# Kernel optimization log

Hardware: AMD Instinct MI355X
Metric: run time of the kernel (lower is better)

The kernel has to match this reference:

```python
import jax, jax.numpy as jnp
import numpy as np

POOL = 7
H, W, C = 200, 200, 512
NUM_ROIS = 128


def setup_inputs() -> dict:
    key = jax.random.key(0)
    k1, k2, k3 = jax.random.split(key, 3)
    img = jax.random.normal(k1, (1, H, W, C), dtype=jnp.float32)
    # (x, y, w, h) in feature-map pixels; w,h >= POOL+1 so every bin is >=1px,
    # and x+w <= W, y+h <= H so crops stay in bounds (as the original assumes).
    wh = jax.random.uniform(k2, (1, NUM_ROIS, 2), minval=float(POOL + 1), maxval=64.0)
    xy = jax.random.uniform(k3, (1, NUM_ROIS, 2)) * (jnp.array([W, H], jnp.float32) - wh)
    rois = jnp.concatenate([xy, wh], axis=-1).astype(jnp.float32)
    return {"img": img, "rois": rois, "pool_size": POOL}


def _roi_pool(x, rois, P):
    # x: (H, W, C) feature map; rois: (R, 4) as (x, y, w, h) floats.
    h_dim, w_dim, _ = x.shape
    ks = jnp.arange(P + 1, dtype=jnp.float32)
    rows = jnp.arange(h_dim)
    cols = jnp.arange(w_dim)

    def pool_one(roi):
        rx, ry, rw, rh = roi[0], roi[1], roi[2], roi[3]
        # Bin boundaries: original computes x1 = int(x + ix*w/P), x2 = int(x + (ix+1)*w/P),
        # i.e. contiguous non-overlapping segments [b[k], b[k+1]).
        bx = (rx + ks * (rw / P)).astype(jnp.int32)
        by = (ry + ks * (rh / P)).astype(jnp.int32)
        # Map each row/col to its bin id; out-of-roi pixels -> dummy segment P.
        rid = jnp.searchsorted(by, rows, side='right') - 1
        rid = jnp.where((rid < 0) | (rid >= P), P, rid)
        cid = jnp.searchsorted(bx, cols, side='right') - 1
        cid = jnp.where((cid < 0) | (cid >= P), P, cid)
        # Max-reduce rows into y-bins, then cols into x-bins (separable rect max).
        rm = jax.ops.segment_max(x, rid, num_segments=P + 1)                     # (P+1, W, C) [jy, w, c]
        cm = jax.ops.segment_max(rm.transpose(1, 0, 2), cid, num_segments=P + 1)  # (P+1, P+1, C) [ix, jy, c]
        return cm[:P, :P].transpose(1, 0, 2)  # (jy, ix, c)

    return jax.vmap(pool_one)(rois)  # (R, P, P, C)


def reference(img, rois, pool_size):
    # Output: (1, num_rois, pool_size, pool_size, channels), tf dim ordering.
    out = _roi_pool(img[0], rois[0], pool_size)
    return out[None]
```

## Files before the change

### kernel.cpp

```cpp
#include <hip/hip_runtime.h>


#define IMG_H 200
#define IMG_W 200
#define IMG_C 512
#define C4 (IMG_C / 4)
#define POOL 7
#define NROI 128
#define PLANES 4
#define NXCD 8
#define NBIN (POOL * POOL)
#define ROIS_PER_XCD (NROI / NXCD)

typedef float f4v __attribute__((ext_vector_type(4)));

__device__ __forceinline__ float4 max4(float4 a, float4 b) {
    return make_float4(fmaxf(a.x, b.x), fmaxf(a.y, b.y),
                       fmaxf(a.z, b.z), fmaxf(a.w, b.w));
}

__device__ __forceinline__ unsigned spread8(unsigned x) {
    x &= 0xFFu;
    x = (x | (x << 4)) & 0x0F0Fu;
    x = (x | (x << 2)) & 0x3333u;
    x = (x | (x << 1)) & 0x5555u;
    return x;
}

__global__ __launch_bounds__(PLANES * 128, 8) void roi_pool_kernel(
    const float* __restrict__ img,
    const float* __restrict__ rois,
    float* __restrict__ out)
{
    __shared__ unsigned short s_key[NROI];
    __shared__ int s_roi;
    __shared__ float4 red[PLANES - 1][C4];

    const int tid = threadIdx.x;

    const int xcd  = blockIdx.x & (NXCD - 1);
    const int ixcd = blockIdx.x >> 3;
    const int rank = xcd * ROIS_PER_XCD + ixcd / NBIN;
    const int bin  = ixcd % NBIN;

    if (tid < NROI) {
        const float rx = rois[tid * 4 + 0];
        const float ry = rois[tid * 4 + 1];
        const float rw = rois[tid * 4 + 2];
        const float rh = rois[tid * 4 + 3];
        const unsigned cx = (unsigned)(int)(rx + 0.5f * rw);
        const unsigned cy = (unsigned)(int)(ry + 0.5f * rh);
        s_key[tid] = (unsigned short)((spread8(cy) << 1) | spread8(cx));
    }
    __syncthreads();
    if (tid < NROI) {
        const unsigned my = s_key[tid];
        int r = 0;
        #pragma unroll 8
        for (int u = 0; u < NROI; ++u) {
            const unsigned ku = s_key[u];
            r += (int)((ku < my) | ((ku == my) & (u < tid)));
        }
        if (r == rank) s_roi = tid;
    }
    __syncthreads();
    const int roi = s_roi;

    const int jy = bin / POOL;
    const int ix = bin % POOL;

    const float rx = rois[roi * 4 + 0];
    const float ry = rois[roi * 4 + 1];
    const float rw = rois[roi * 4 + 2];
    const float rh = rois[roi * 4 + 3];

    const float sx = __fdiv_rn(rw, 7.0f);
    const float sy = __fdiv_rn(rh, 7.0f);
    const int x1 = (int)__fadd_rn(rx, __fmul_rn((float)ix,       sx));
    const int x2 = (int)__fadd_rn(rx, __fmul_rn((float)(ix + 1), sx));
    const int y1 = (int)__fadd_rn(ry, __fmul_rn((float)jy,       sy));
    const int y2 = (int)__fadd_rn(ry, __fmul_rn((float)(jy + 1), sy));

    const int c4 = tid & 127;
    const int p  = tid >> 7;
    const float4* __restrict__ img4 = (const float4*)img;

    const int bw = x2 - x1;
    const int bh = y2 - y1;
    const int area = bw * bh;
    (void)bh;

    const float4 NEG = make_float4(-INFINITY, -INFINITY, -INFINITY, -INFINITY);
    float4 m = NEG;

    int dx = p, dy = 0;
    while (dx >= bw) { dx -= bw; ++dy; }
    #pragma unroll 2
    for (int i = p; i < area; i += PLANES) {
        const size_t px = (size_t)(y1 + dy) * IMG_W + (size_t)(x1 + dx);
        m = max4(m, img4[px * C4 + c4]);
        dx += PLANES;
        while (dx >= bw) { dx -= bw; ++dy; }
    }

    if (p > 0) red[p - 1][c4] = m;
    __syncthreads();
    if (p == 0) {
        m = max4(m, red[0][c4]);
        m = max4(m, red[1][c4]);
        m = max4(m, red[2][c4]);

        float4* __restrict__ out4 = (float4*)out;
        f4v* __restrict__ dst =
            (f4v*)&out4[((size_t)(roi * POOL + jy) * POOL + ix) * C4 + c4];
        __builtin_nontemporal_store(*(const f4v*)&m, dst);
    }
}

extern "C" void kernel_launch(void* const* d_in, const int* in_sizes, int n_in,
                              void* d_out, int out_size, void* d_ws, size_t ws_size,
                              hipStream_t stream) {
    (void)in_sizes; (void)n_in; (void)d_ws; (void)ws_size; (void)out_size;
    const float* img  = (const float*)d_in[0];
    const float* rois = (const float*)d_in[1];
    float* out = (float*)d_out;

    dim3 grid(NROI * NBIN);
    dim3 block(PLANES * 128);
    roi_pool_kernel<<<grid, block, 0, stream>>>(img, rois, out);
}
```

Measured before the change: 153.1 us.

## Balance ROI work across XCDs by area-weighted Morton-ordered chunking

Result: faster. 145.1 us (-5.2%).

```diff
diff --git a/kernel.cpp b/kernel.cpp
--- a/kernel.cpp
+++ b/kernel.cpp
@@ -10,7 +10,8 @@
 #define PLANES 4
 #define NXCD 8
 #define NBIN (POOL * POOL)
-#define ROIS_PER_XCD (NROI / NXCD)
+#define NITEM (NROI * NBIN)
+#define SLOTS_PER_XCD (NITEM / NXCD)
 
 typedef float f4v __attribute__((ext_vector_type(4)));
 
@@ -18,6 +19,9 @@
     return make_float4(fmaxf(a.x, b.x), fmaxf(a.y, b.y),
                        fmaxf(a.z, b.z), fmaxf(a.w, b.w));
 }
+
+__device__ __forceinline__ int imin(int a, int b) { return a < b ? a : b; }
+__device__ __forceinline__ int imax(int a, int b) { return a > b ? a : b; }
 
 __device__ __forceinline__ unsigned spread8(unsigned x) {
     x &= 0xFFu;
@@ -33,39 +37,119 @@
     float* __restrict__ out)
 {
     __shared__ unsigned short s_key[NROI];
-    __shared__ int s_roi;
-    __shared__ float4 red[PLANES - 1][C4];
+    __shared__ float          s_areaROI[NROI];
+    __shared__ int            s_rank[NROI];
+    __shared__ unsigned char  s_perm[NROI];
+    __shared__ float          s_area[NROI];
+    __shared__ float          s_pref[NROI];
+    __shared__ int            s_chunk[NROI];
+    __shared__ int            s_rstart[NXCD];
+    __shared__ int            s_len[NXCD];
+    __shared__ int            s_spillpre[NXCD + 1];
+    __shared__ int            s_freepre[NXCD + 1];
+    __shared__ int            s_roi, s_bin;
+    __shared__ float4         red[PLANES - 1][C4];
 
     const int tid = threadIdx.x;
-
-    const int xcd  = blockIdx.x & (NXCD - 1);
-    const int ixcd = blockIdx.x >> 3;
-    const int rank = xcd * ROIS_PER_XCD + ixcd / NBIN;
-    const int bin  = ixcd % NBIN;
-
-    if (tid < NROI) {
-        const float rx = rois[tid * 4 + 0];
-        const float ry = rois[tid * 4 + 1];
-        const float rw = rois[tid * 4 + 2];
-        const float rh = rois[tid * 4 + 3];
+    const int t   = tid & 127;
+    const int seg = tid >> 7;
+
+    if (seg == 0) {
+        const float rx = rois[t * 4 + 0];
+        const float ry = rois[t * 4 + 1];
+        const float rw = rois[t * 4 + 2];
+        const float rh = rois[t * 4 + 3];
         const unsigned cx = (unsigned)(int)(rx + 0.5f * rw);
         const unsigned cy = (unsigned)(int)(ry + 0.5f * rh);
-        s_key[tid] = (unsigned short)((spread8(cy) << 1) | spread8(cx));
-    }
-    __syncthreads();
-    if (tid < NROI) {
-        const unsigned my = s_key[tid];
+        s_key[t] = (unsigned short)((spread8(cy) << 1) | spread8(cx));
+        s_areaROI[t] = rw * rh;
+        s_rank[t] = 0;
+    }
+    if (tid < NXCD) s_len[tid] = 0;
+    __syncthreads();
+
+    {
+        const unsigned my = s_key[t];
         int r = 0;
+        const int u0 = seg * 32;
         #pragma unroll 8
-        for (int u = 0; u < NROI; ++u) {
+        for (int u = u0; u < u0 + 32; ++u) {
             const unsigned ku = s_key[u];
-            r += (int)((ku < my) | ((ku == my) & (u < tid)));
-        }
-        if (r == rank) s_roi = tid;
-    }
-    __syncthreads();
+            r += (int)((ku < my) | ((ku == my) & (u < t)));
+        }
+        atomicAdd(&s_rank[t], r);
+    }
+    __syncthreads();
+
+    if (seg == 0) {
+        const int r = s_rank[t];
+        s_perm[r] = (unsigned char)t;
+        s_area[r] = s_areaROI[t];
+    }
+    __syncthreads();
+
+    if (seg == 0) {
+        float v = s_area[t];
+        #pragma unroll
+        for (int d = 1; d < 64; d <<= 1) {
+            const float o = __shfl_up(v, d);
+            if ((t & 63) >= d) v += o;
+        }
+        s_pref[t] = v;
+    }
+    __syncthreads();
+
+    if (seg == 0) {
+        const float w0tot = s_pref[63];
+        const float pre   = s_pref[t] + ((t >= 64) ? w0tot : 0.f);
+        const float total = s_pref[127] + w0tot;
+        const float mid = pre - 0.5f * s_area[t];
+        const int c = imin((int)(mid * ((float)NXCD / total)), NXCD - 1);
+        s_chunk[t] = c;
+        atomicAdd(&s_len[c], NBIN);
+    }
+    __syncthreads();
+
+    if (seg == 0) {
+        const int c = s_chunk[t];
+        if (t == 0 || s_chunk[t - 1] != c) s_rstart[c] = t;
+    }
+    if (tid == 0) {
+        int sp = 0, fp = 0;
+        #pragma unroll
+        for (int x = 0; x < NXCD; ++x) {
+            s_spillpre[x] = sp;
+            s_freepre[x]  = fp;
+            sp += imax(0, s_len[x] - SLOTS_PER_XCD);
+            fp += imax(0, SLOTS_PER_XCD - s_len[x]);
+        }
+        s_spillpre[NXCD] = sp;
+        s_freepre[NXCD]  = fp;
+    }
+    __syncthreads();
+
+    if (tid == 0) {
+        const int x = blockIdx.x & (NXCD - 1);
+        const int j = blockIdx.x >> 3;
+        int tt, mm;
+        if (j < s_len[x]) {
+            tt = s_rstart[x] + j / NBIN;
+            mm = j % NBIN;
+        } else {
+            const int si = s_freepre[x] + (j - s_len[x]);
+            int xx = 0;
+            while (!(si >= s_spillpre[xx] && si < s_spillpre[xx + 1])) ++xx;
+            const int jj = SLOTS_PER_XCD + (si - s_spillpre[xx]);
+            tt = s_rstart[xx] + jj / NBIN;
+            mm = jj % NBIN;
+        }
+        s_roi = (int)s_perm[tt];
+        s_bin = mm;
+    }
+    __syncthreads();
+
     const int roi = s_roi;
-
+    const int bin = s_bin;
     const int jy = bin / POOL;
     const int ix = bin % POOL;
 
@@ -86,9 +170,7 @@
     const float4* __restrict__ img4 = (const float4*)img;
 
     const int bw = x2 - x1;
-    const int bh = y2 - y1;
-    const int area = bw * bh;
-    (void)bh;
+    const int area = bw * (y2 - y1);
 
     const float4 NEG = make_float4(-INFINITY, -INFINITY, -INFINITY, -INFINITY);
     float4 m = NEG;
@@ -125,7 +207,6 @@
     const float* rois = (const float*)d_in[1];
     float* out = (float*)d_out;
 
-    dim3 grid(NROI * NBIN);
-    dim3 block(PLANES * 128);
-    roi_pool_kernel<<<grid, block, 0, stream>>>(img, rois, out);
-}
+    roi_pool_kernel<<<dim3(NITEM), dim3(PLANES * 128), 0, stream>>>(
+        img, rois, out);
+}
```
